# Kernel tuning notes

Hardware: AMD Instinct MI355X
Metric: run time of the kernel (lower is better)

## Reference

```python
import jax, jax.numpy as jnp
import numpy as np

N_NODES = 100000
N_EDGES = 1600000
C = 128            # in_channels
NB = 32            # num_bundles
NUM_ATT = 4
TIME_STEPS = (1, 2, 4, 8)


def setup_inputs() -> dict:
    key = jax.random.key(0)
    ks = jax.random.split(key, 8)
    x = jax.random.normal(ks[0], (N_NODES, C), dtype=jnp.float32)
    edge_index = jax.random.randint(ks[1], (2, N_EDGES), 0, N_NODES, dtype=jnp.int64)
    lin_w = jax.random.normal(ks[2], (C, C), dtype=jnp.float32) / np.sqrt(C)
    lin_b = jnp.zeros((C,), dtype=jnp.float32)
    enc_w1 = jax.random.normal(ks[3], (C, 2 * NB), dtype=jnp.float32) / np.sqrt(C)
    enc_b1 = jnp.zeros((2 * NB,), dtype=jnp.float32)
    enc_w2 = jax.random.normal(ks[4], (2 * NB, NB), dtype=jnp.float32) / np.sqrt(2 * NB)
    enc_b2 = jnp.zeros((NB,), dtype=jnp.float32)
    attention = jax.random.uniform(ks[5], (NUM_ATT, NB), dtype=jnp.float32)
    return {"x": x, "edge_index": edge_index, "lin_w": lin_w, "lin_b": lin_b,
            "enc_w1": enc_w1, "enc_b1": enc_b1, "enc_w2": enc_w2, "enc_b2": enc_b2,
            "attention": attention}


def _forward(x, edge_index, lin_w, lin_b, enc_w1, enc_b1, enc_w2, enc_b2, attention):
    N = x.shape[0]
    # --- normalization: add self loops, edge_weight = 1/deg[target] ---
    sl = jnp.arange(N, dtype=edge_index.dtype)
    src = jnp.concatenate([edge_index[0], sl])   # message source (x_j)
    dst = jnp.concatenate([edge_index[1], sl])   # aggregation target
    deg = jax.ops.segment_sum(jnp.ones_like(src, dtype=x.dtype), src, num_segments=N)
    ew = (1.0 / deg)[dst]                        # [E+N]

    # --- struct_enc MLP -> per-bundle rotation angles ---
    hmid = jax.nn.gelu(x @ enc_w1 + enc_b1, approximate=False)
    theta = jnp.pi * jnp.tanh(hmid @ enc_w2 + enc_b2)   # [N, NB], euler angles
    c, s = jnp.cos(theta), jnp.sin(theta)
    # R[n,b] = [[c,-s],[s,c]] : [N, NB, 2, 2]
    R = jnp.stack([jnp.stack([c, -s], axis=-1), jnp.stack([s, c], axis=-1)], axis=-2)

    # --- rotate vector field, linear map ---
    vf = x.reshape(N, NB, 2, -1)                          # [N, NB, 2, d]
    vf = jnp.einsum('nbij,nbjd->nbid', R, vf)
    h = vf.reshape(N, C) @ lin_w + lin_b

    # --- multi-hop propagation, store states at checkpoints ---
    def prop(hh):
        msg = hh[src] * ew[:, None]                       # gather + weight
        return jax.ops.segment_sum(msg, dst, num_segments=N)

    stored = []
    t = 0
    for ts in TIME_STEPS:
        for _ in range(ts - t):
            h = prop(h)
        t = ts
        stored.append(h)
    dt = jnp.stack(stored)                                # [num_att, N, C]

    # --- attention-weighted time combine ---
    att = jax.nn.softmax(attention, axis=0)               # [num_att, NB]
    dt = dt.reshape(NUM_ATT, N, NB, -1)
    h = jnp.einsum('ab,anbd->nbd', att, dt)               # [N, NB, 2*d]

    # --- inverse (transpose) rotation ---
    vf = h.reshape(N, NB, 2, -1)
    vf = jnp.einsum('nbji,nbjd->nbid', R, vf)             # R^T @ v
    h = vf.reshape(N, C)

    return x + h  # residual (dropout p=0, batchnorm off)


def reference(x, edge_index, lin_w, lin_b, enc_w1, enc_b1, enc_w2, enc_b2, attention):
    return _forward(x, edge_index, lin_w, lin_b, enc_w1, enc_b1, enc_w2, enc_b2, attention)
```

## Files before the change

### kernel.cpp

```cpp
#include <hip/hip_runtime.h>
#include <math.h>

typedef unsigned int uint;


__device__ __forceinline__ float bf_lo(uint u) { return __uint_as_float(u << 16); }
__device__ __forceinline__ float bf_hi(uint u) { return __uint_as_float(u & 0xFFFF0000u); }
__device__ __forceinline__ uint pack_bf16(float x, float y) {
    uint ux = __float_as_uint(x), uy = __float_as_uint(y);
    ux += 0x7FFFu + ((ux >> 16) & 1u);
    uy += 0x7FFFu + ((uy >> 16) & 1u);
    return (ux >> 16) | (uy & 0xFFFF0000u);
}

#define BK 64
#define SBLK 64


__global__ void init_k(int* cnt, int* deg, int* cursor, int n) {
    int i = blockIdx.x * 256 + threadIdx.x;
    if (i < n) { cnt[i] = 0; deg[i] = 1; }
    if (blockIdx.x == 0 && threadIdx.x == 0) cursor[0] = 0;
}


__global__ __launch_bounds__(256) void build_shard_k(
    const int* __restrict__ src, const int* __restrict__ dst,
    int* cnt, int* deg, int* __restrict__ csr, int E, int N)
{
    const int myshard = blockIdx.x & 7;
    const int nps = (N + 7) >> 3;
    const int lo = myshard * nps;
    const int hi = (lo + nps < N) ? lo + nps : N;
    const int stride = (gridDim.x >> 3) * 256;
    for (int e = (blockIdx.x >> 3) * 256 + threadIdx.x; e < E; e += stride) {
        int d = __builtin_nontemporal_load(dst + e);
        int s = __builtin_nontemporal_load(src + e);
        if (d >= lo && d < hi) {
            int p = atomicAdd(&cnt[d], 1);
            if (p < BK) csr[(size_t)d * BK + p] = s;
        }
        if (s >= lo && s < hi) atomicAdd(&deg[s], 1);
    }
}


__global__ void count_k(const int* __restrict__ src, const int* __restrict__ dst,
                        int* cnt, int* deg, int E) {
    int e = blockIdx.x * 256 + threadIdx.x;
    if (e < E) {
        atomicAdd(&cnt[dst[e]], 1);
        atomicAdd(&deg[src[e]], 1);
    }
}

__global__ void alloc_k(const int* __restrict__ cnt, int* off, int* fil, int* cursor, int n) {
    int i = blockIdx.x * 256 + threadIdx.x;
    if (i < n) {
        off[i] = atomicAdd(cursor, cnt[i]);
        fil[i] = 0;
    }
}

__global__ void fill_k(const int* __restrict__ src, const int* __restrict__ dst,
                       const int* __restrict__ off, int* fil, int* csr, int E) {
    int e = blockIdx.x * 256 + threadIdx.x;
    if (e < E) {
        int d = dst[e];
        int p = atomicAdd(&fil[d], 1);
        csr[off[d] + p] = src[e];
    }
}


__global__ void post_k(const int* __restrict__ deg, float* invdeg, int n) {
    int i = blockIdx.x * 256 + threadIdx.x;
    if (i < n) invdeg[i] = 1.0f / (float)deg[i];
}


__global__ __launch_bounds__(256) void blockhist_k(const int* __restrict__ cnt,
                                                   int* __restrict__ blockHist, int n) {
    __shared__ int lh[64];
    if (threadIdx.x < 64) lh[threadIdx.x] = 0;
    __syncthreads();
    for (int i = blockIdx.x * 256 + threadIdx.x; i < n; i += gridDim.x * 256) {
        int b = cnt[i]; if (b > 63) b = 63;
        atomicAdd(&lh[b], 1);
    }
    __syncthreads();
    if (threadIdx.x < 64) blockHist[threadIdx.x * SBLK + blockIdx.x] = lh[threadIdx.x];
}

__global__ void scan2_k(int* __restrict__ blockHist) {
    __shared__ int binTotal[64];
    __shared__ int binStart[64];
    int b = threadIdx.x;
    if (b < 64) {
        int s = 0;
        for (int k = 0; k < SBLK; k++) {
            int v = blockHist[b * SBLK + k];
            blockHist[b * SBLK + k] = s;
            s += v;
        }
        binTotal[b] = s;
    }
    __syncthreads();
    if (threadIdx.x == 0) {
        int s = 0;
        for (int bb = 0; bb < 64; bb++) { binStart[bb] = s; s += binTotal[bb]; }
    }
    __syncthreads();
    if (b < 64) {
        int add = binStart[b];
        for (int k = 0; k < SBLK; k++) blockHist[b * SBLK + k] += add;
    }
}

__global__ __launch_bounds__(256) void scatter2_k(const int* __restrict__ cnt,
                                                  const int* __restrict__ blockHist,
                                                  int* __restrict__ perm, int n) {
    __shared__ int lbase[64];
    if (threadIdx.x < 64) lbase[threadIdx.x] = blockHist[threadIdx.x * SBLK + blockIdx.x];
    __syncthreads();
    for (int i = blockIdx.x * 256 + threadIdx.x; i < n; i += gridDim.x * 256) {
        int b = cnt[i]; if (b > 63) b = 63;
        int pos = atomicAdd(&lbase[b], 1);
        perm[pos] = i;
    }
}


__global__ void att_k(const float* __restrict__ att, float* att_sm) {
    int b = threadIdx.x;
    if (b < 32) {
        float v0 = att[b], v1 = att[32 + b], v2 = att[64 + b], v3 = att[96 + b];
        float m = fmaxf(fmaxf(v0, v1), fmaxf(v2, v3));
        float e0 = expf(v0 - m), e1 = expf(v1 - m), e2 = expf(v2 - m), e3 = expf(v3 - m);
        float inv = 1.0f / (e0 + e1 + e2 + e3);
        att_sm[b] = e0 * inv; att_sm[32 + b] = e1 * inv;
        att_sm[64 + b] = e2 * inv; att_sm[96 + b] = e3 * inv;
    }
}


__global__ __launch_bounds__(256) void angles_k(
    const float* __restrict__ x,
    const float* __restrict__ w1, const float* __restrict__ b1,
    const float* __restrict__ w2, const float* __restrict__ b2,
    uint* __restrict__ cs_out, int n_nodes, int n_tiles)
{
    __shared__ float s_w1[128 * 64];
    __shared__ float s_w2[64 * 32];
    __shared__ float s_x[32 * 128];
    __shared__ float s_h[32 * 64];
    const int t = threadIdx.x;

    for (int i = t; i < 128 * 64 / 4; i += 256) ((float4*)s_w1)[i] = ((const float4*)w1)[i];
    for (int i = t; i < 64 * 32 / 4; i += 256)  ((float4*)s_w2)[i] = ((const float4*)w2)[i];

    for (int tile = blockIdx.x; tile < n_tiles; tile += gridDim.x) {
        const int base = tile * 32;
        __syncthreads();
        for (int i = t; i < 32 * 32; i += 256) {
            int r = i >> 5, q = i & 31;
            int n = base + r;
            float4 v = make_float4(0.f, 0.f, 0.f, 0.f);
            if (n < n_nodes) v = ((const float4*)x)[(size_t)n * 32 + q];
            ((float4*)&s_x[r * 128])[q] = v;
        }
        __syncthreads();
        {
            const int tx = t & 15, ty = t >> 4;
            float4 bv = ((const float4*)b1)[tx];
            float acc[2][4];
            #pragma unroll
            for (int i = 0; i < 2; i++) { acc[i][0] = bv.x; acc[i][1] = bv.y; acc[i][2] = bv.z; acc[i][3] = bv.w; }
            for (int k = 0; k < 128; k++) {
                float4 w = ((float4*)s_w1)[k * 16 + tx];
                #pragma unroll
                for (int i = 0; i < 2; i++) {
                    float xv = s_x[(ty * 2 + i) * 128 + k];
                    acc[i][0] += xv * w.x; acc[i][1] += xv * w.y;
                    acc[i][2] += xv * w.z; acc[i][3] += xv * w.w;
                }
            }
            #pragma unroll
            for (int i = 0; i < 2; i++)
                #pragma unroll
                for (int j = 0; j < 4; j++) {
                    float v = acc[i][j];
                    s_h[(ty * 2 + i) * 64 + tx * 4 + j] = 0.5f * v * (1.0f + erff(v * 0.70710678118654752f));
                }
        }
        __syncthreads();
        {
            const int tx = t & 7, ty = t >> 3;
            float4 bv = ((const float4*)b2)[tx];
            float acc[4] = {bv.x, bv.y, bv.z, bv.w};
            for (int k = 0; k < 64; k++) {
                float4 w = ((float4*)s_w2)[k * 8 + tx];
                float hv = s_h[ty * 64 + k];
                acc[0] += hv * w.x; acc[1] += hv * w.y;
                acc[2] += hv * w.z; acc[3] += hv * w.w;
            }
            int n = base + ty;
            if (n < n_nodes) {
                uint4 pk;
                float c, s, th;
                th = 3.14159265358979323846f * tanhf(acc[0]); sincosf(th, &s, &c); pk.x = pack_bf16(c, s);
                th = 3.14159265358979323846f * tanhf(acc[1]); sincosf(th, &s, &c); pk.y = pack_bf16(c, s);
                th = 3.14159265358979323846f * tanhf(acc[2]); sincosf(th, &s, &c); pk.z = pack_bf16(c, s);
                th = 3.14159265358979323846f * tanhf(acc[3]); sincosf(th, &s, &c); pk.w = pack_bf16(c, s);
                ((uint4*)&cs_out[(size_t)n * 32])[tx] = pk;
            }
        }
    }
}


__global__ __launch_bounds__(256) void rotlin_k(
    const float* __restrict__ x, const uint* __restrict__ cs,
    const float* __restrict__ lin_w, const float* __restrict__ lin_b,
    uint* __restrict__ h0, int n_nodes, int n_tiles)
{
    __shared__ float s_lw[128 * 128];
    __shared__ float s_x[32 * 128];
    const int t = threadIdx.x;

    for (int i = t; i < 128 * 128 / 4; i += 256) ((float4*)s_lw)[i] = ((const float4*)lin_w)[i];

    for (int tile = blockIdx.x; tile < n_tiles; tile += gridDim.x) {
        const int base = tile * 32;
        __syncthreads();
        for (int i = t; i < 32 * 32; i += 256) {
            int r = i >> 5, q = i & 31;
            int n = base + r;
            float4 v = make_float4(0.f, 0.f, 0.f, 0.f);
            if (n < n_nodes) v = ((const float4*)x)[(size_t)n * 32 + q];
            ((float4*)&s_x[r * 128])[q] = v;
        }
        __syncthreads();
        for (int i = t; i < 32 * 32; i += 256) {
            int r = i >> 5, b = i & 31;
            int n = base + r;
            if (n < n_nodes) {
                uint csu = cs[(size_t)n * 32 + b];
                float c = bf_lo(csu), s = bf_hi(csu);
                float* xr = &s_x[r * 128 + b * 4];
                float v00 = xr[0], v01 = xr[1], v10 = xr[2], v11 = xr[3];
                xr[0] = c * v00 - s * v10;
                xr[1] = c * v01 - s * v11;
                xr[2] = s * v00 + c * v10;
                xr[3] = s * v01 + c * v11;
            }
        }
        __syncthreads();
        {
            const int tx = t & 31, ty = t >> 5;
            float4 bv = ((const float4*)lin_b)[tx];
            float acc[4][4];
            #pragma unroll
            for (int i = 0; i < 4; i++) { acc[i][0] = bv.x; acc[i][1] = bv.y; acc[i][2] = bv.z; acc[i][3] = bv.w; }
            for (int k = 0; k < 128; k++) {
                float4 w = ((float4*)s_lw)[k * 32 + tx];
                #pragma unroll
                for (int i = 0; i < 4; i++) {
                    float xv = s_x[(ty * 4 + i) * 128 + k];
                    acc[i][0] += xv * w.x; acc[i][1] += xv * w.y;
                    acc[i][2] += xv * w.z; acc[i][3] += xv * w.w;
                }
            }
            #pragma unroll
            for (int i = 0; i < 4; i++) {
                int n = base + ty * 4 + i;
                if (n < n_nodes) {
                    uint2 pk;
                    pk.x = pack_bf16(acc[i][0], acc[i][1]);
                    pk.y = pack_bf16(acc[i][2], acc[i][3]);
                    ((uint2*)&h0[(size_t)n * 64])[tx] = pk;
                }
            }
        }
    }
}


__global__ __launch_bounds__(256) void prop64_k(
    const uint* __restrict__ hin, uint* __restrict__ hout,
    const int* __restrict__ csr, const int* __restrict__ off,
    const int* __restrict__ cnt, const float* __restrict__ invdeg, int maxc,
    const float* __restrict__ att_sm, int att_row, float* __restrict__ acc,
    int init_acc, int n_nodes)
{
    int gw = (int)((blockIdx.x * 256 + threadIdx.x) >> 6);
    int lane = threadIdx.x & 63;
    if (gw >= n_nodes) return;
    int c = cnt[gw]; if (c > maxc) c = maxc;
    size_t o = off ? (size_t)off[gw] : (size_t)gw * BK;
    size_t selfidx = (size_t)gw * 64 + lane;
    uint su = hin[selfidx];
    float ax = bf_lo(su), ay = bf_hi(su);
    int j = 0;
    for (; j + 8 <= c; j += 8) {
        int s0 = csr[o + j + 0], s1 = csr[o + j + 1], s2 = csr[o + j + 2], s3 = csr[o + j + 3];
        int s4 = csr[o + j + 4], s5 = csr[o + j + 5], s6 = csr[o + j + 6], s7 = csr[o + j + 7];
        uint v0 = hin[(size_t)s0 * 64 + lane];
        uint v1 = hin[(size_t)s1 * 64 + lane];
        uint v2 = hin[(size_t)s2 * 64 + lane];
        uint v3 = hin[(size_t)s3 * 64 + lane];
        uint v4 = hin[(size_t)s4 * 64 + lane];
        uint v5 = hin[(size_t)s5 * 64 + lane];
        uint v6 = hin[(size_t)s6 * 64 + lane];
        uint v7 = hin[(size_t)s7 * 64 + lane];
        ax += ((bf_lo(v0) + bf_lo(v1)) + (bf_lo(v2) + bf_lo(v3)))
            + ((bf_lo(v4) + bf_lo(v5)) + (bf_lo(v6) + bf_lo(v7)));
        ay += ((bf_hi(v0) + bf_hi(v1)) + (bf_hi(v2) + bf_hi(v3)))
            + ((bf_hi(v4) + bf_hi(v5)) + (bf_hi(v6) + bf_hi(v7)));
    }
    for (; j < c; ++j) {
        int s = csr[o + j];
        uint v = hin[(size_t)s * 64 + lane];
        ax += bf_lo(v); ay += bf_hi(v);
    }
    float id = invdeg[gw];
    ax *= id; ay *= id;
    hout[selfidx] = pack_bf16(ax, ay);
    if (att_row >= 0) {
        float wv = att_sm[att_row * 32 + (lane >> 1)];
        float2* a2 = (float2*)acc;
        float2 res = make_float2(wv * ax, wv * ay);
        if (!init_acc) { float2 p = a2[selfidx]; res.x += p.x; res.y += p.y; }
        a2[selfidx] = res;
    }
}


__global__ __launch_bounds__(256) void prop16_k(
    const uint* __restrict__ hin, uint* __restrict__ hout,
    const int* __restrict__ csr, const int* __restrict__ off,
    const int* __restrict__ cnt, const float* __restrict__ invdeg,
    const int* __restrict__ perm, int maxc,
    const float* __restrict__ att_sm, int att_row, float* __restrict__ acc,
    int init_acc, int n_nodes)
{
    int tid = blockIdx.x * 256 + threadIdx.x;
    int wid = tid >> 6;
    int lane = threadIdx.x & 63;
    int g = lane >> 4, l16 = lane & 15;
    int pos = wid * 4 + g;
    bool valid = pos < n_nodes;
    int node = valid ? perm[pos] : 0;
    int myCnt = valid ? cnt[node] : 0;
    if (myCnt > maxc) myCnt = maxc;
    size_t o = off ? (size_t)(valid ? off[node] : 0) : (size_t)node * BK;
    float id = valid ? invdeg[node] : 0.f;

    const uint4* h4 = (const uint4*)hin;
    uint4 sv = valid ? h4[(size_t)node * 16 + l16] : make_uint4(0, 0, 0, 0);
    float a0 = bf_lo(sv.x), a1 = bf_hi(sv.x), a2 = bf_lo(sv.y), a3 = bf_hi(sv.y);
    float a4 = bf_lo(sv.z), a5 = bf_hi(sv.z), a6 = bf_lo(sv.w), a7 = bf_hi(sv.w);

    int cm = myCnt;
    cm = max(cm, __shfl_xor(cm, 16));
    cm = max(cm, __shfl_xor(cm, 32));

    #pragma unroll 4
    for (int j = 0; j < cm; ++j) {
        if (j < myCnt) {
            int s = csr[o + j];
            uint4 v = h4[(size_t)s * 16 + l16];
            a0 += bf_lo(v.x); a1 += bf_hi(v.x);
            a2 += bf_lo(v.y); a3 += bf_hi(v.y);
            a4 += bf_lo(v.z); a5 += bf_hi(v.z);
            a6 += bf_lo(v.w); a7 += bf_hi(v.w);
        }
    }
    if (!valid) return;
    a0 *= id; a1 *= id; a2 *= id; a3 *= id;
    a4 *= id; a5 *= id; a6 *= id; a7 *= id;
    uint4 pk;
    pk.x = pack_bf16(a0, a1); pk.y = pack_bf16(a2, a3);
    pk.z = pack_bf16(a4, a5); pk.w = pack_bf16(a6, a7);
    ((uint4*)hout)[(size_t)node * 16 + l16] = pk;
    if (att_row >= 0) {
        float wv0 = att_sm[att_row * 32 + l16 * 2];
        float wv1 = att_sm[att_row * 32 + l16 * 2 + 1];
        float4* ap = (float4*)acc;
        size_t bidx = (size_t)node * 32 + l16 * 2;
        float4 r0 = make_float4(wv0 * a0, wv0 * a1, wv0 * a2, wv0 * a3);
        float4 r1 = make_float4(wv1 * a4, wv1 * a5, wv1 * a6, wv1 * a7);
        if (!init_acc) {
            float4 p0 = ap[bidx], p1 = ap[bidx + 1];
            r0.x += p0.x; r0.y += p0.y; r0.z += p0.z; r0.w += p0.w;
            r1.x += p1.x; r1.y += p1.y; r1.z += p1.z; r1.w += p1.w;
        }
        ap[bidx] = r0; ap[bidx + 1] = r1;
    }
}


__global__ __launch_bounds__(256) void final2_k(
    const float* __restrict__ x, const uint* __restrict__ cs,
    const uint* __restrict__ c1, const uint* __restrict__ c2,
    const uint* __restrict__ c4, const uint* __restrict__ c8,
    const float* __restrict__ att_sm, float* __restrict__ out, int n_nodes)
{
    __shared__ float s_att[128];
    int t = threadIdx.x;
    if (t < 128) s_att[t] = att_sm[t];
    __syncthreads();
    int i = blockIdx.x * 256 + t;
    if (i >= n_nodes * 32) return;
    int b = i & 31;
    uint2 u1 = ((const uint2*)c1)[i];
    uint2 u2 = ((const uint2*)c2)[i];
    uint2 u4 = ((const uint2*)c4)[i];
    uint2 u8 = ((const uint2*)c8)[i];
    float w0 = s_att[b], w1 = s_att[32 + b], w2 = s_att[64 + b], w3 = s_att[96 + b];
    float h0 = w0 * bf_lo(u1.x) + w1 * bf_lo(u2.x) + w2 * bf_lo(u4.x) + w3 * bf_lo(u8.x);
    float h1 = w0 * bf_hi(u1.x) + w1 * bf_hi(u2.x) + w2 * bf_hi(u4.x) + w3 * bf_hi(u8.x);
    float h2 = w0 * bf_lo(u1.y) + w1 * bf_lo(u2.y) + w2 * bf_lo(u4.y) + w3 * bf_lo(u8.y);
    float h3 = w0 * bf_hi(u1.y) + w1 * bf_hi(u2.y) + w2 * bf_hi(u4.y) + w3 * bf_hi(u8.y);
    uint csu = cs[i];
    float c = bf_lo(csu), s = bf_hi(csu);
    float4 xv = ((const float4*)x)[i];
    ((float4*)out)[i] = make_float4(
        xv.x + ( c * h0 + s * h2),
        xv.y + ( c * h1 + s * h3),
        xv.z + (-s * h0 + c * h2),
        xv.w + (-s * h1 + c * h3));
}

__global__ __launch_bounds__(256) void final_k(
    const float* __restrict__ x, const uint* __restrict__ cs,
    float* __restrict__ out, int n_nodes)
{
    int i = blockIdx.x * 256 + threadIdx.x;
    if (i >= n_nodes * 32) return;
    uint csu = cs[i];
    float c = bf_lo(csu), s = bf_hi(csu);
    float4 v = ((float4*)out)[i];
    float4 xv = ((const float4*)x)[i];
    ((float4*)out)[i] = make_float4(
        xv.x + ( c * v.x + s * v.z),
        xv.y + ( c * v.y + s * v.w),
        xv.z + (-s * v.x + c * v.z),
        xv.w + (-s * v.y + c * v.w));
}


extern "C" void kernel_launch(void* const* d_in, const int* in_sizes, int n_in,
                              void* d_out, int out_size, void* d_ws, size_t ws_size,
                              hipStream_t stream) {
    const float* x     = (const float*)d_in[0];
    const int*   ei    = (const int*)d_in[1];
    const float* lin_w = (const float*)d_in[2];
    const float* lin_b = (const float*)d_in[3];
    const float* w1    = (const float*)d_in[4];
    const float* b1    = (const float*)d_in[5];
    const float* w2    = (const float*)d_in[6];
    const float* b2    = (const float*)d_in[7];
    const float* att   = (const float*)d_in[8];
    const int N = in_sizes[0] / 128;
    const int E = in_sizes[1] / 2;
    const int* srcp = ei;
    const int* dstp = ei + E;
    float* out = (float*)d_out;

    char* w = (char*)d_ws;
    size_t used = 0;
    auto walloc = [&](size_t bytes) {
        char* p = w; size_t a = (bytes + 255) & ~255UL; w += a; used += a; return p;
    };
    int*   cnt       = (int*)walloc((size_t)N * 4);
    int*   deg       = (int*)walloc((size_t)N * 4);
    float* invdeg    = (float*)walloc((size_t)N * 4);
    int*   perm      = (int*)walloc((size_t)N * 4);
    int*   blockHist = (int*)walloc(64 * SBLK * 4);
    int*   cursor    = (int*)walloc(256);
    float* att_sm    = (float*)walloc(512);
    uint*  cs        = (uint*)walloc((size_t)N * 32 * 4);

    size_t bufBytes  = (size_t)N * 64 * 4;
    size_t bucketB   = (size_t)N * BK * 4;
    size_t remain = (ws_size > used) ? (ws_size - used) : 0;
    bool big = remain >= bucketB + 5 * bufBytes + 4096;
    bool mid = !big && remain >= bucketB + 2 * bufBytes + 4096;

    int nb_n = (N + 255) / 256;
    int nb_e = (E + 255) / 256;
    int n_tiles = (N + 31) / 32;
    int pb64 = (N * 64 + 255) / 256;
    int pb16 = ((N + 3) / 4 + 3) / 4;
    int fb = (N * 32 + 255) / 256;

    hipLaunchKernelGGL(init_k, dim3(nb_n), dim3(256), 0, stream, cnt, deg, cursor, N);

    const int* offp = nullptr;
    int* csr;
    int maxc;
    if (big || mid) {
        csr = (int*)walloc(bucketB);
        maxc = BK;
        hipLaunchKernelGGL(build_shard_k, dim3(1024), dim3(256), 0, stream,
                           srcp, dstp, cnt, deg, csr, E, N);
    } else {
        int* off = (int*)walloc((size_t)N * 4);
        int* fil = (int*)walloc((size_t)N * 4);
        csr = (int*)walloc((size_t)E * 4);
        maxc = 1 << 30;
        offp = off;
        hipLaunchKernelGGL(count_k, dim3(nb_e), dim3(256), 0, stream, srcp, dstp, cnt, deg, E);
        hipLaunchKernelGGL(alloc_k, dim3(nb_n), dim3(256), 0, stream, cnt, off, fil, cursor, N);
        hipLaunchKernelGGL(fill_k,  dim3(nb_e), dim3(256), 0, stream, srcp, dstp, off, fil, csr, E);
    }
    hipLaunchKernelGGL(post_k,      dim3(nb_n), dim3(256), 0, stream, deg, invdeg, N);
    hipLaunchKernelGGL(blockhist_k, dim3(SBLK), dim3(256), 0, stream, cnt, blockHist, N);
    hipLaunchKernelGGL(scan2_k,     dim3(1),    dim3(64),  0, stream, blockHist);
    hipLaunchKernelGGL(scatter2_k,  dim3(SBLK), dim3(256), 0, stream, cnt, blockHist, perm, N);
    hipLaunchKernelGGL(att_k,       dim3(1),    dim3(64),  0, stream, att, att_sm);

    if (big) {
        uint* T0 = (uint*)walloc(bufBytes);
        uint* C1 = (uint*)walloc(bufBytes);
        uint* C2 = (uint*)walloc(bufBytes);
        uint* C4 = (uint*)walloc(bufBytes);
        uint* C8 = (uint*)walloc(bufBytes);

        hipLaunchKernelGGL(angles_k, dim3(512), dim3(256), 0, stream,
                           x, w1, b1, w2, b2, cs, N, n_tiles);
        hipLaunchKernelGGL(rotlin_k, dim3(512), dim3(256), 0, stream,
                           x, cs, lin_w, lin_b, T0, N, n_tiles);

        uint* seq_in [8] = {T0, C1, C2, T0, C4, T0, C8, T0};
        uint* seq_out[8] = {C1, C2, T0, C4, T0, C8, T0, C8};
        for (int step = 0; step < 8; ++step) {
            if ((step & 1) == 0) {
                hipLaunchKernelGGL(prop64_k, dim3(pb64), dim3(256), 0, stream,
                                   seq_in[step], seq_out[step], csr, offp, cnt, invdeg,
                                   maxc, att_sm, -1, out, 0, N);
            } else {
                hipLaunchKernelGGL(prop16_k, dim3(pb16), dim3(256), 0, stream,
                                   seq_in[step], seq_out[step], csr, offp, cnt, invdeg,
                                   perm, maxc, att_sm, -1, out, 0, N);
            }
        }
        hipLaunchKernelGGL(final2_k, dim3(fb), dim3(256), 0, stream,
                           x, cs, C1, C2, C4, C8, att_sm, out, N);
    } else {
        uint* bufA = (uint*)walloc(bufBytes);
        uint* bufB = (uint*)walloc(bufBytes);

        hipLaunchKernelGGL(angles_k, dim3(512), dim3(256), 0, stream,
                           x, w1, b1, w2, b2, cs, N, n_tiles);
        hipLaunchKernelGGL(rotlin_k, dim3(512), dim3(256), 0, stream,
                           x, cs, lin_w, lin_b, bufA, N, n_tiles);

        int ckpt[9] = {-1, 0, 1, -1, 2, -1, -1, -1, 3};
        uint* hi = bufA; uint* ho = bufB;
        for (int step = 1; step <= 8; ++step) {
            hipLaunchKernelGGL(prop64_k, dim3(pb64), dim3(256), 0, stream,
                               hi, ho, csr, offp, cnt, invdeg, maxc,
                               att_sm, ckpt[step], out, (step == 1) ? 1 : 0, N);
            uint* tmp = hi; hi = ho; ho = tmp;
        }
        hipLaunchKernelGGL(final_k, dim3(fb), dim3(256), 0, stream, x, cs, out, N);
    }
}
```

Before: 932.3 us.

## Partition edges by shard before bucket CSR build and compute degrees in LDS

Adds a new default path that first partitions edges into per-block, per-shard queues, then builds the bucketed CSR from those queues. Previously each shard block scanned all edges. Degrees come from a per-shard shared-memory histogram instead of global atomics. A specialised prop64 kernel loads neighbour indices as int4 and unrolls the gather by 16. Risks: queues are capped at QCAP per block and shard, so an overflow would silently drop edges, and the degree pass runs on only 8 blocks.

```diff
diff --git a/kernel.cpp b/kernel.cpp
--- a/kernel.cpp
+++ b/kernel.cpp
@@ -15,12 +15,91 @@
 
 #define BK 64
 #define SBLK 64
-
+#define PBLK 256
+#define QCAP 1024
+#define MAXNPS 12544
+
+
+__global__ void init0_k(int* cnt, int n) {
+    int i = blockIdx.x * 256 + threadIdx.x;
+    if (i < n) cnt[i] = 0;
+}
 
 __global__ void init_k(int* cnt, int* deg, int* cursor, int n) {
     int i = blockIdx.x * 256 + threadIdx.x;
     if (i < n) { cnt[i] = 0; deg[i] = 1; }
     if (blockIdx.x == 0 && threadIdx.x == 0) cursor[0] = 0;
+}
+
+
+__global__ __launch_bounds__(256) void partition_k(
+    const int* __restrict__ src, const int* __restrict__ dst,
+    int2* __restrict__ qpair, int* __restrict__ qcnt,
+    int* __restrict__ q2, int* __restrict__ q2cnt,
+    int E, int nps)
+{
+    __shared__ int lcnt[8], l2cnt[8];
+    if (threadIdx.x < 8) { lcnt[threadIdx.x] = 0; l2cnt[threadIdx.x] = 0; }
+    __syncthreads();
+    int ch = (E + PBLK - 1) / PBLK;
+    int lo = blockIdx.x * ch;
+    int hi = min(E, lo + ch);
+    for (int e = lo + threadIdx.x; e < hi; e += 256) {
+        int s = src[e], d = dst[e];
+        int sh = d / nps;
+        int lp = atomicAdd(&lcnt[sh], 1);
+        if (lp < QCAP)
+            qpair[((size_t)blockIdx.x * 8 + sh) * QCAP + lp] = make_int2(s, d);
+        int sh2 = s / nps;
+        int l2p = atomicAdd(&l2cnt[sh2], 1);
+        if (l2p < QCAP)
+            q2[((size_t)blockIdx.x * 8 + sh2) * QCAP + l2p] = s;
+    }
+    __syncthreads();
+    if (threadIdx.x < 8) {
+        qcnt[blockIdx.x * 8 + threadIdx.x] = min(lcnt[threadIdx.x], QCAP);
+        q2cnt[blockIdx.x * 8 + threadIdx.x] = min(l2cnt[threadIdx.x], QCAP);
+    }
+}
+
+
+__global__ __launch_bounds__(256) void build2_k(
+    const int2* __restrict__ qpair, const int* __restrict__ qcnt,
+    int* cnt, int* __restrict__ csr)
+{
+    int shard = blockIdx.x & 7;
+    int r = blockIdx.x >> 3;
+    for (int pb = r; pb < PBLK; pb += 128) {
+        int base = (pb * 8 + shard) * QCAP;
+        int n = qcnt[pb * 8 + shard];
+        for (int i = threadIdx.x; i < n; i += 256) {
+            int2 pr = qpair[base + i];
+            int p = atomicAdd(&cnt[pr.y], 1);
+            if (p < BK) csr[(size_t)pr.y * BK + p] = pr.x;
+        }
+    }
+}
+
+
+__global__ __launch_bounds__(256) void deg_k(
+    const int* __restrict__ q2, const int* __restrict__ q2cnt,
+    float* __restrict__ invdeg, int nps, int N)
+{
+    __shared__ int hist[MAXNPS];
+    int shard = blockIdx.x;
+    int lo = shard * nps;
+    int nn = min(nps, N - lo);
+    for (int i = threadIdx.x; i < nn; i += 256) hist[i] = 0;
+    __syncthreads();
+    for (int pb = 0; pb < PBLK; ++pb) {
+        int base = (pb * 8 + shard) * QCAP;
+        int n = q2cnt[pb * 8 + shard];
+        for (int i = threadIdx.x; i < n; i += 256)
+            atomicAdd(&hist[q2[base + i] - lo], 1);
+    }
+    __syncthreads();
+    for (int i = threadIdx.x; i < nn; i += 256)
+        invdeg[lo + i] = 1.0f / (float)(hist[i] + 1);
 }
 
 
@@ -71,7 +150,6 @@
         csr[off[d] + p] = src[e];
     }
 }
-
 
 __global__ void post_k(const int* __restrict__ deg, float* invdeg, int n) {
     int i = blockIdx.x * 256 + threadIdx.x;
@@ -288,6 +366,78 @@
 
 __global__ __launch_bounds__(256) void prop64_k(
     const uint* __restrict__ hin, uint* __restrict__ hout,
+    const int* __restrict__ csr, const int* __restrict__ cnt,
+    const float* __restrict__ invdeg,
+    const float* __restrict__ att_sm, int att_row, float* __restrict__ acc,
+    int init_acc, int n_nodes)
+{
+    int gw = (int)((blockIdx.x * 256 + threadIdx.x) >> 6);
+    int lane = threadIdx.x & 63;
+    if (gw >= n_nodes) return;
+    int c = cnt[gw]; if (c > BK) c = BK;
+    const int* cp = csr + (size_t)gw * BK;
+    size_t selfidx = (size_t)gw * 64 + lane;
+    uint su = hin[selfidx];
+    float ax = bf_lo(su), ay = bf_hi(su);
+    int j = 0;
+    for (; j + 16 <= c; j += 16) {
+        int4 i0 = *(const int4*)(cp + j);
+        int4 i1 = *(const int4*)(cp + j + 4);
+        int4 i2 = *(const int4*)(cp + j + 8);
+        int4 i3 = *(const int4*)(cp + j + 12);
+        uint v0  = hin[(size_t)i0.x * 64 + lane];
+        uint v1  = hin[(size_t)i0.y * 64 + lane];
+        uint v2  = hin[(size_t)i0.z * 64 + lane];
+        uint v3  = hin[(size_t)i0.w * 64 + lane];
+        uint v4  = hin[(size_t)i1.x * 64 + lane];
+        uint v5  = hin[(size_t)i1.y * 64 + lane];
+        uint v6  = hin[(size_t)i1.z * 64 + lane];
+        uint v7  = hin[(size_t)i1.w * 64 + lane];
+        uint v8  = hin[(size_t)i2.x * 64 + lane];
+        uint v9  = hin[(size_t)i2.y * 64 + lane];
+        uint v10 = hin[(size_t)i2.z * 64 + lane];
+        uint v11 = hin[(size_t)i2.w * 64 + lane];
+        uint v12 = hin[(size_t)i3.x * 64 + lane];
+        uint v13 = hin[(size_t)i3.y * 64 + lane];
+        uint v14 = hin[(size_t)i3.z * 64 + lane];
+        uint v15 = hin[(size_t)i3.w * 64 + lane];
+        ax += (((bf_lo(v0) + bf_lo(v1)) + (bf_lo(v2) + bf_lo(v3)))
+             + ((bf_lo(v4) + bf_lo(v5)) + (bf_lo(v6) + bf_lo(v7))))
+            + (((bf_lo(v8) + bf_lo(v9)) + (bf_lo(v10) + bf_lo(v11)))
+             + ((bf_lo(v12) + bf_lo(v13)) + (bf_lo(v14) + bf_lo(v15))));
+        ay += (((bf_hi(v0) + bf_hi(v1)) + (bf_hi(v2) + bf_hi(v3)))
+             + ((bf_hi(v4) + bf_hi(v5)) + (bf_hi(v6) + bf_hi(v7))))
+            + (((bf_hi(v8) + bf_hi(v9)) + (bf_hi(v10) + bf_hi(v11)))
+             + ((bf_hi(v12) + bf_hi(v13)) + (bf_hi(v14) + bf_hi(v15))));
+    }
+    for (; j + 4 <= c; j += 4) {
+        int4 ii = *(const int4*)(cp + j);
+        uint v0 = hin[(size_t)ii.x * 64 + lane];
+        uint v1 = hin[(size_t)ii.y * 64 + lane];
+        uint v2 = hin[(size_t)ii.z * 64 + lane];
+        uint v3 = hin[(size_t)ii.w * 64 + lane];
+        ax += (bf_lo(v0) + bf_lo(v1)) + (bf_lo(v2) + bf_lo(v3));
+        ay += (bf_hi(v0) + bf_hi(v1)) + (bf_hi(v2) + bf_hi(v3));
+    }
+    for (; j < c; ++j) {
+        int s = cp[j];
+        uint v = hin[(size_t)s * 64 + lane];
+        ax += bf_lo(v); ay += bf_hi(v);
+    }
+    float id = invdeg[gw];
+    ax *= id; ay *= id;
+    hout[selfidx] = pack_bf16(ax, ay);
+    if (att_row >= 0) {
+        float wv = att_sm[att_row * 32 + (lane >> 1)];
+        float2* a2 = (float2*)acc;
+        float2 res = make_float2(wv * ax, wv * ay);
+        if (!init_acc) { float2 p = a2[selfidx]; res.x += p.x; res.y += p.y; }
+        a2[selfidx] = res;
+    }
+}
+
+__global__ __launch_bounds__(256) void prop64f_k(
+    const uint* __restrict__ hin, uint* __restrict__ hout,
     const int* __restrict__ csr, const int* __restrict__ off,
     const int* __restrict__ cnt, const float* __restrict__ invdeg, int maxc,
     const float* __restrict__ att_sm, int att_row, float* __restrict__ acc,
@@ -467,6 +617,7 @@
     const int* srcp = ei;
     const int* dstp = ei + E;
     float* out = (float*)d_out;
+    const int nps = (N + 7) / 8;
 
     char* w = (char*)d_ws;
     size_t used = 0;
@@ -474,7 +625,6 @@
         char* p = w; size_t a = (bytes + 255) & ~255UL; w += a; used += a; return p;
     };
     int*   cnt       = (int*)walloc((size_t)N * 4);
-    int*   deg       = (int*)walloc((size_t)N * 4);
     float* invdeg    = (float*)walloc((size_t)N * 4);
     int*   perm      = (int*)walloc((size_t)N * 4);
     int*   blockHist = (int*)walloc(64 * SBLK * 4);
@@ -482,11 +632,18 @@
     float* att_sm    = (float*)walloc(512);
     uint*  cs        = (uint*)walloc((size_t)N * 32 * 4);
 
-    size_t bufBytes  = (size_t)N * 64 * 4;
-    size_t bucketB   = (size_t)N * BK * 4;
+    size_t bufBytes = (size_t)N * 64 * 4;
+    size_t bucketB  = (size_t)N * BK * 4;
+    size_t qpairB   = (size_t)PBLK * 8 * QCAP * 8;
+    size_t q2B      = (size_t)PBLK * 8 * QCAP * 4;
+    size_t qcntB    = (size_t)PBLK * 8 * 4;
     size_t remain = (ws_size > used) ? (ws_size - used) : 0;
-    bool big = remain >= bucketB + 5 * bufBytes + 4096;
-    bool mid = !big && remain >= bucketB + 2 * bufBytes + 4096;
+
+    bool huge = (nps <= MAXNPS) &&
+                remain >= bucketB + qpairB + q2B + 2 * qcntB + 5 * bufBytes + 65536;
+    bool big  = !huge && remain >= bucketB + (size_t)N * 4 + 5 * bufBytes + 65536;
+    bool mid  = !huge && !big &&
+                remain >= bucketB + (size_t)N * 4 + 2 * bufBytes + 65536;
 
     int nb_n = (N + 255) / 256;
     int nb_e = (E + 255) / 256;
@@ -495,6 +652,54 @@
     int pb16 = ((N + 3) / 4 + 3) / 4;
     int fb = (N * 32 + 255) / 256;
 
+    if (huge) {
+        int*  csr    = (int*)walloc(bucketB);
+        int2* qpair  = (int2*)walloc(qpairB);
+        int*  qcnt   = (int*)walloc(qcntB);
+        int*  q2     = (int*)walloc(q2B);
+        int*  q2cnt  = (int*)walloc(qcntB);
+        uint* T0 = (uint*)walloc(bufBytes);
+        uint* C1 = (uint*)walloc(bufBytes);
+        uint* C2 = (uint*)walloc(bufBytes);
+        uint* C4 = (uint*)walloc(bufBytes);
+        uint* C8 = (uint*)walloc(bufBytes);
+
+        hipLaunchKernelGGL(init0_k,     dim3(nb_n), dim3(256), 0, stream, cnt, N);
+        hipLaunchKernelGGL(partition_k, dim3(PBLK), dim3(256), 0, stream,
+                           srcp, dstp, qpair, qcnt, q2, q2cnt, E, nps);
+        hipLaunchKernelGGL(build2_k,    dim3(1024), dim3(256), 0, stream,
+                           qpair, qcnt, cnt, csr);
+        hipLaunchKernelGGL(deg_k,       dim3(8),    dim3(256), 0, stream,
+                           q2, q2cnt, invdeg, nps, N);
+        hipLaunchKernelGGL(blockhist_k, dim3(SBLK), dim3(256), 0, stream, cnt, blockHist, N);
+        hipLaunchKernelGGL(scan2_k,     dim3(1),    dim3(64),  0, stream, blockHist);
+        hipLaunchKernelGGL(scatter2_k,  dim3(SBLK), dim3(256), 0, stream, cnt, blockHist, perm, N);
+        hipLaunchKernelGGL(att_k,       dim3(1),    dim3(64),  0, stream, att, att_sm);
+
+        hipLaunchKernelGGL(angles_k, dim3(512), dim3(256), 0, stream,
+                           x, w1, b1, w2, b2, cs, N, n_tiles);
+        hipLaunchKernelGGL(rotlin_k, dim3(512), dim3(256), 0, stream,
+                           x, cs, lin_w, lin_b, T0, N, n_tiles);
+
+        uint* seq_in [8] = {T0, C1, C2, T0, C4, T0, C8, T0};
+        uint* seq_out[8] = {C1, C2, T0, C4, T0, C8, T0, C8};
+        for (int step = 0; step < 8; ++step) {
+            if ((step & 1) == 0) {
+                hipLaunchKernelGGL(prop64_k, dim3(pb64), dim3(256), 0, stream,
+                                   seq_in[step], seq_out[step], csr, cnt, invdeg,
+                                   att_sm, -1, out, 0, N);
+            } else {
+                hipLaunchKernelGGL(prop16_k, dim3(pb16), dim3(256), 0, stream,
+                                   seq_in[step], seq_out[step], csr, nullptr, cnt, invdeg,
+                                   perm, BK, att_sm, -1, out, 0, N);
+            }
+        }
+        hipLaunchKernelGGL(final2_k, dim3(fb), dim3(256), 0, stream,
+                           x, cs, C1, C2, C4, C8, att_sm, out, N);
+        return;
+    }
+
+    int* deg = (int*)walloc((size_t)N * 4);
     hipLaunchKernelGGL(init_k, dim3(nb_n), dim3(256), 0, stream, cnt, deg, cursor, N);
 
     const int* offp = nullptr;
@@ -515,11 +720,8 @@
         hipLaunchKernelGGL(alloc_k, dim3(nb_n), dim3(256), 0, stream, cnt, off, fil, cursor, N);
         hipLaunchKernelGGL(fill_k,  dim3(nb_e), dim3(256), 0, stream, srcp, dstp, off, fil, csr, E);
     }
-    hipLaunchKernelGGL(post_k,      dim3(nb_n), dim3(256), 0, stream, deg, invdeg, N);
-    hipLaunchKernelGGL(blockhist_k, dim3(SBLK), dim3(256), 0, stream, cnt, blockHist, N);
-    hipLaunchKernelGGL(scan2_k,     dim3(1),    dim3(64),  0, stream, blockHist);
-    hipLaunchKernelGGL(scatter2_k,  dim3(SBLK), dim3(256), 0, stream, cnt, blockHist, perm, N);
-    hipLaunchKernelGGL(att_k,       dim3(1),    dim3(64),  0, stream, att, att_sm);
+    hipLaunchKernelGGL(post_k, dim3(nb_n), dim3(256), 0, stream, deg, invdeg, N);
+    hipLaunchKernelGGL(att_k,  dim3(1),    dim3(64),  0, stream, att, att_sm);
 
     if (big) {
         uint* T0 = (uint*)walloc(bufBytes);
@@ -536,15 +738,9 @@
         uint* seq_in [8] = {T0, C1, C2, T0, C4, T0, C8, T0};
         uint* seq_out[8] = {C1, C2, T0, C4, T0, C8, T0, C8};
         for (int step = 0; step < 8; ++step) {
-            if ((step & 1) == 0) {
-                hipLaunchKernelGGL(prop64_k, dim3(pb64), dim3(256), 0, stream,
-                                   seq_in[step], seq_out[step], csr, offp, cnt, invdeg,
-                                   maxc, att_sm, -1, out, 0, N);
-            } else {
-                hipLaunchKernelGGL(prop16_k, dim3(pb16), dim3(256), 0, stream,
-                                   seq_in[step], seq_out[step], csr, offp, cnt, invdeg,
-                                   perm, maxc, att_sm, -1, out, 0, N);
-            }
+            hipLaunchKernelGGL(prop64f_k, dim3(pb64), dim3(256), 0, stream,
+                               seq_in[step], seq_out[step], csr, offp, cnt, invdeg,
+                               maxc, att_sm, -1, out, 0, N);
         }
         hipLaunchKernelGGL(final2_k, dim3(fb), dim3(256), 0, stream,
                            x, cs, C1, C2, C4, C8, att_sm, out, N);
@@ -560,7 +756,7 @@
         int ckpt[9] = {-1, 0, 1, -1, 2, -1, -1, -1, 3};
         uint* hi = bufA; uint* ho = bufB;
         for (int step = 1; step <= 8; ++step) {
-            hipLaunchKernelGGL(prop64_k, dim3(pb64), dim3(256), 0, stream,
+            hipLaunchKernelGGL(prop64f_k, dim3(pb64), dim3(256), 0, stream,
                                hi, ho, csr, offp, cnt, invdeg, maxc,
                                att_sm, ckpt[step], out, (step == 1) ? 1 : 0, N);
             uint* tmp = hi; hi = ho; ho = tmp;
```

After: 1.132 ms. 21.4% more time.
